# Optimization experiments

Measured on AMD Instinct MI355X. Metric: run time of the kernel, lower is better.

## Reference

```python
import jax, jax.numpy as jnp
import numpy as np

HIDDEN = 2048
N_HEADS = 16
HEAD_DIM = HIDDEN // N_HEADS  # 128
GROUP_SIZE = 128
ROPE_THETA = 10000.0
EPS = 1e-8
THRESH = 0.5


def ternary_quantize_groupwise(w):
    O, I = w.shape
    wg = w.reshape(O, I // GROUP_SIZE, GROUP_SIZE)
    scale = jnp.maximum(jnp.mean(jnp.abs(wg), axis=-1, keepdims=True), EPS)
    wn = wg / scale
    q = jnp.where(wn > THRESH, 1.0, jnp.where(wn < -THRESH, -1.0, 0.0))
    return (q * scale).reshape(O, I)


def quantize_with_ste(w):
    wq = ternary_quantize_groupwise(w)
    return w + jax.lax.stop_gradient(wq - w)


def rope_tables(seqlen):
    half = HEAD_DIM // 2
    inv_freq = 1.0 / (ROPE_THETA ** (jnp.arange(half, dtype=jnp.float32) / half))
    freqs = jnp.arange(seqlen, dtype=jnp.float32)[:, None] * inv_freq[None, :]  # [S, half]
    return jnp.cos(freqs), jnp.sin(freqs)


def apply_rope(x, cos, sin):
    # x: [B, H, S, D]; cos/sin: [S, D/2]
    d = x.shape[-1]
    x1, x2 = x[..., : d // 2], x[..., d // 2:]
    c = cos[None, None, :, :].astype(x.dtype)
    s = sin[None, None, :, :].astype(x.dtype)
    return jnp.concatenate([x1 * c - x2 * s, x1 * s + x2 * c], axis=-1)


def setup_inputs() -> dict:
    key = jax.random.key(0)
    ks = jax.random.split(key, 5)
    B, S = 1, 2048
    hidden_states = jax.random.normal(ks[0], (B, S, HIDDEN), dtype=jnp.float32)
    attention_mask = jnp.ones((B, S), dtype=jnp.int32)
    init_scale = 1.0 / np.sqrt(HIDDEN)
    wq = jax.random.normal(ks[1], (HIDDEN, HIDDEN), dtype=jnp.float32) * init_scale
    wk = jax.random.normal(ks[2], (HIDDEN, HIDDEN), dtype=jnp.float32) * init_scale
    wv = jax.random.normal(ks[3], (HIDDEN, HIDDEN), dtype=jnp.float32) * init_scale
    wo = jax.random.normal(ks[4], (HIDDEN, HIDDEN), dtype=jnp.float32) * init_scale
    return {"hidden_states": hidden_states, "attention_mask": attention_mask,
            "wq": wq, "wk": wk, "wv": wv, "wo": wo}


def reference(hidden_states, attention_mask, wq, wk, wv, wo):
    B, S, _ = hidden_states.shape
    cos, sin = rope_tables(S)

    def proj(x, w):
        w_q = quantize_with_ste(w)
        y = jnp.einsum('bsi,oi->bso', x, w_q)
        return y.reshape(B, S, N_HEADS, HEAD_DIM).transpose(0, 2, 1, 3)  # [B,H,S,D]

    q = apply_rope(proj(hidden_states, wq), cos, sin)
    k = apply_rope(proj(hidden_states, wk), cos, sin)
    v = proj(hidden_states, wv)

    scores = jnp.einsum('bhsd,bhtd->bhst', q, k) / np.sqrt(HEAD_DIM)
    causal = jnp.triu(jnp.ones((S, S), dtype=bool), k=1)
    scores = jnp.where(causal[None, None, :, :], -jnp.inf, scores)
    pad = (attention_mask == 0)[:, None, None, :]
    scores = jnp.where(pad, -jnp.inf, scores)

    probs = jax.nn.softmax(scores, axis=-1)
    out = jnp.einsum('bhst,bhtd->bhsd', probs, v)
    out = out.transpose(0, 2, 1, 3).reshape(B, S, HIDDEN)

    wo_q = quantize_with_ste(wo)
    return jnp.einsum('bso,po->bsp', out, wo_q)
```

## Files before the change

### kernel.cpp

```cpp
#include <hip/hip_runtime.h>
#include <cstdint>
#include <cstddef>


typedef __attribute__((ext_vector_type(8))) short bf16x8;
typedef __attribute__((ext_vector_type(4))) float f32x4;
typedef __attribute__((address_space(3))) void lds_void;
typedef const __attribute__((address_space(1))) void gmem_void;

__device__ __forceinline__ short f2bf(float x) {
    union { float f; uint32_t u; } c; c.f = x;
    uint32_t r = (c.u + 0x7FFFu + ((c.u >> 16) & 1u)) >> 16;
    return (short)r;
}
__device__ __forceinline__ float bf2f(short x) {
    union { uint32_t u; float f; } c; c.u = ((uint32_t)(uint16_t)x) << 16;
    return c.f;
}

__global__ __launch_bounds__(64) void zero_flag(int* f) {
    if (threadIdx.x == 0) *f = 0;
}

__global__ __launch_bounds__(256) void detect_kernel(
    const unsigned short* __restrict__ p, int n, int* __restrict__ flag)
{
    int tid = blockIdx.x * 256 + threadIdx.x;
    int cnt = 0;
    for (int i = tid; i < n; i += 65536) {
        int e = (p[i] >> 7) & 0xFF;
        cnt += (e >= 0xF0) ? 1 : 0;
    }
#pragma unroll
    for (int off = 1; off < 64; off <<= 1) cnt += __shfl_xor(cnt, off);
    if ((threadIdx.x & 63) == 0 && cnt) atomicAdd(flag, cnt);
}

__global__ __launch_bounds__(256) void convert_kernel(
    const void* __restrict__ in, short* __restrict__ out, int n,
    const int* __restrict__ flag)
{
    bool isf32 = (*flag > 1000);
    int i = (blockIdx.x * 256 + threadIdx.x) * 4;
    if (i >= n) return;
    if (isf32) {
        float4 v = *(const float4*)((const float*)in + i);
        short4 o;
        o.x = f2bf(v.x); o.y = f2bf(v.y); o.z = f2bf(v.z); o.w = f2bf(v.w);
        *(short4*)(out + i) = o;
    } else {
        *(short4*)(out + i) = *(const short4*)((const short*)in + i);
    }
}

__global__ __launch_bounds__(256) void quant_kernel(
    const void* __restrict__ w0, const void* __restrict__ w1,
    const void* __restrict__ w2, const void* __restrict__ w3,
    short* __restrict__ q0, short* __restrict__ q1,
    short* __restrict__ q2, short* __restrict__ q3,
    const int* __restrict__ flag)
{
    bool isf32 = (*flag > 1000);
    int gw   = blockIdx.x * 4 + (threadIdx.x >> 6);
    int lane = threadIdx.x & 63;
    int mat  = gw >> 15;
    int g    = gw & 32767;
    const void* w = (mat == 0) ? w0 : (mat == 1) ? w1 : (mat == 2) ? w2 : w3;
    short*      q = (mat == 0) ? q0 : (mat == 1) ? q1 : (mat == 2) ? q2 : q3;
    int idx = g * 64 + lane;
    float a, b;
    if (isf32) {
        const float* wf = (const float*)w;
        a = wf[idx * 2]; b = wf[idx * 2 + 1];
    } else {
        int pr = ((const int*)w)[idx];
        a = bf2f((short)(pr & 0xFFFF));
        b = bf2f((short)(((uint32_t)pr) >> 16));
    }
    float s = fabsf(a) + fabsf(b);
#pragma unroll
    for (int off = 1; off < 64; off <<= 1) s += __shfl_xor(s, off);
    float scale = fmaxf(s * (1.0f / 128.0f), 1e-8f);
    float na = a / scale, nb = b / scale;
    float ra = (na > 0.5f) ? scale : (na < -0.5f) ? -scale : 0.0f;
    float rb = (nb > 0.5f) ? scale : (nb < -0.5f) ? -scale : 0.0f;
    ((int*)q)[idx] = (int)(uint16_t)f2bf(ra) | ((int)(uint16_t)f2bf(rb) << 16);
}

__global__ __launch_bounds__(512, 2) void gemm_qkv(
    const short* __restrict__ A, const short* __restrict__ B,
    short* __restrict__ C)
{
    __shared__ short lds[32768];
    short* A0 = lds;          short* A1 = lds + 8192;
    short* B0 = lds + 16384;  short* B1 = lds + 24576;

    int wg = blockIdx.y * 24 + blockIdx.x;
    int sw = (wg & 7) * 24 + (wg >> 3);
    int bx = sw % 24, by = sw / 24;

    const short* Ab = A + (long long)by * 256 * 2048;
    const short* Bb = B + (long long)bx * 256 * 2048;

    int tid = threadIdx.x, lane = tid & 63, wid = tid >> 6;
    int wr = wid >> 2, wc = wid & 3;
    int quad = lane >> 4, lm = lane & 15;

    f32x4 acc[8][4];
#pragma unroll
    for (int i = 0; i < 8; i++)
#pragma unroll
        for (int j = 0; j < 4; j++)
#pragma unroll
            for (int r = 0; r < 4; r++) acc[i][j][r] = 0.0f;

    auto stage = [&](int tn, short* dA, short* dB) {
#pragma unroll
        for (int l = 0; l < 2; l++) {
            int ci = l * 512 + tid;
            int R = ci >> 2;
            int kc = ((ci & 3) - (R >> 1)) & 3;
            const short* gp = Ab + (long long)R * 2048 + tn * 32 + kc * 8;
            __builtin_amdgcn_global_load_lds((gmem_void*)gp, (lds_void*)(dA + ci * 8), 16, 0, 0);
        }
#pragma unroll
        for (int l = 0; l < 2; l++) {
            int ci = l * 512 + tid;
            int R = ci >> 2;
            int kc = ((ci & 3) - (R >> 1)) & 3;
            const short* gp = Bb + (long long)R * 2048 + tn * 32 + kc * 8;
            __builtin_amdgcn_global_load_lds((gmem_void*)gp, (lds_void*)(dB + ci * 8), 16, 0, 0);
        }
    };

    auto tile = [&](short* cA, short* cB, short* nA, short* nB, int tn, bool pf) {
        if (pf) stage(tn, nA, nB);
        bf16x8 af[4], bg[4];
#pragma unroll
        for (int m = 0; m < 4; m++) {
            int R = wr * 128 + m * 16 + lm;
            af[m] = *(const bf16x8*)(cA + R * 32 + (((quad + (R >> 1)) & 3) << 3));
        }
#pragma unroll
        for (int n = 0; n < 4; n++) {
            int R = wc * 64 + n * 16 + lm;
            bg[n] = *(const bf16x8*)(cB + R * 32 + (((quad + (R >> 1)) & 3) << 3));
        }
        __builtin_amdgcn_s_barrier();
        __builtin_amdgcn_s_setprio(1);
#pragma unroll
        for (int m = 0; m < 4; m++)
#pragma unroll
            for (int n = 0; n < 4; n++)
                acc[m][n] = __builtin_amdgcn_mfma_f32_16x16x32_bf16(af[m], bg[n], acc[m][n], 0, 0, 0);
        __builtin_amdgcn_s_setprio(0);
        __builtin_amdgcn_s_barrier();
#pragma unroll
        for (int m = 0; m < 4; m++) {
            int R = wr * 128 + 64 + m * 16 + lm;
            af[m] = *(const bf16x8*)(cA + R * 32 + (((quad + (R >> 1)) & 3) << 3));
        }
        __builtin_amdgcn_s_barrier();
        __builtin_amdgcn_s_setprio(1);
#pragma unroll
        for (int m = 0; m < 4; m++)
#pragma unroll
            for (int n = 0; n < 4; n++)
                acc[m + 4][n] = __builtin_amdgcn_mfma_f32_16x16x32_bf16(af[m], bg[n], acc[m + 4][n], 0, 0, 0);
        __builtin_amdgcn_s_setprio(0);
        if (pf) asm volatile("s_waitcnt vmcnt(0)" ::: "memory");
        __builtin_amdgcn_s_barrier();
    };

    stage(0, A0, B0);
    asm volatile("s_waitcnt vmcnt(0)" ::: "memory");
    __syncthreads();

    for (int t = 0; t < 64; t += 2) {
        tile(A0, B0, A1, B1, t + 1, true);
        tile(A1, B1, A0, B0, t + 2, t + 2 < 64);
    }

#pragma unroll
    for (int m = 0; m < 8; m++)
#pragma unroll
        for (int n = 0; n < 4; n++)
#pragma unroll
            for (int r = 0; r < 4; r++) {
                int row = by * 256 + wr * 128 + m * 16 + quad * 4 + r;
                int col = bx * 256 + wc * 64 + n * 16 + lm;
                C[(long long)row * 6144 + col] = f2bf(acc[m][n][r]);
            }
}

__global__ __launch_bounds__(256) void vtrans_kernel(
    const short* __restrict__ qkv, short* __restrict__ v_t)
{
    __shared__ short lt[4096];
    int bt = blockIdx.x, bo = blockIdx.y;
    int tid = threadIdx.x;
    int r = tid >> 3, c = tid & 7;
#pragma unroll
    for (int h = 0; h < 2; h++) {
        int row = h * 32 + r;
        bf16x8 v = *(const bf16x8*)(qkv + (long long)(bt * 64 + row) * 6144 + 4096 + bo * 64 + c * 8);
        *(bf16x8*)(lt + row * 64 + ((c ^ (row & 7)) << 3)) = v;
    }
    __syncthreads();
#pragma unroll
    for (int h = 0; h < 2; h++) {
        int o = h * 32 + r;
        bf16x8 ov;
#pragma unroll
        for (int k = 0; k < 8; k++) {
            int row = c * 8 + k;
            ov[k] = lt[row * 64 + ((((o >> 3) ^ (row & 7))) << 3) + (o & 7)];
        }
        *(bf16x8*)(v_t + (long long)(bo * 64 + o) * 2048 + bt * 64 + c * 8) = ov;
    }
}

__global__ __launch_bounds__(256) void gemm_wo(
    const short* __restrict__ A, const short* __restrict__ B,
    float* __restrict__ C)
{
    int bx = blockIdx.x, by = blockIdx.y;
    const short* Ab = A + (long long)by * 128 * 2048;
    const short* Bb = B + (long long)bx * 64 * 2048;
    __shared__ short lA[128 * 64];
    __shared__ short lB[64 * 64];
    int tid = threadIdx.x;
    int lane = tid & 63, wv = tid >> 6;
    f32x4 acc[2][4];
#pragma unroll
    for (int i = 0; i < 2; i++)
#pragma unroll
        for (int j = 0; j < 4; j++)
#pragma unroll
            for (int r = 0; r < 4; r++) acc[i][j][r] = 0.0f;

    int rbase = wv * 32;

    for (int k0 = 0; k0 < 2048; k0 += 64) {
        __syncthreads();
#pragma unroll
        for (int i = 0; i < 4; i++) {
            int ci  = i * 256 + tid;
            int row = ci >> 3;
            int kcG = (ci & 7) ^ (row & 7);
            const short* gp = Ab + (long long)row * 2048 + k0 + kcG * 8;
            __builtin_amdgcn_global_load_lds((gmem_void*)gp, (lds_void*)(lA + ci * 8), 16, 0, 0);
        }
#pragma unroll
        for (int i = 0; i < 2; i++) {
            int ci  = i * 256 + tid;
            int row = ci >> 3;
            int kcG = (ci & 7) ^ (row & 7);
            const short* gp = Bb + (long long)row * 2048 + k0 + kcG * 8;
            __builtin_amdgcn_global_load_lds((gmem_void*)gp, (lds_void*)(lB + ci * 8), 16, 0, 0);
        }
        __syncthreads();
#pragma unroll
        for (int kk = 0; kk < 2; kk++) {
            int kc = kk * 4 + (lane >> 4);
            bf16x8 a[2], b[4];
#pragma unroll
            for (int t = 0; t < 2; t++) {
                int r = rbase + t * 16 + (lane & 15);
                a[t] = *(const bf16x8*)(lA + (r * 8 + (kc ^ (r & 7))) * 8);
            }
#pragma unroll
            for (int t = 0; t < 4; t++) {
                int r = t * 16 + (lane & 15);
                b[t] = *(const bf16x8*)(lB + (r * 8 + (kc ^ (r & 7))) * 8);
            }
#pragma unroll
            for (int mt = 0; mt < 2; mt++)
#pragma unroll
                for (int nt = 0; nt < 4; nt++)
                    acc[mt][nt] = __builtin_amdgcn_mfma_f32_16x16x32_bf16(a[mt], b[nt], acc[mt][nt], 0, 0, 0);
        }
    }

    int rq = (lane >> 4) * 4, cq = lane & 15;
#pragma unroll
    for (int mt = 0; mt < 2; mt++)
#pragma unroll
        for (int nt = 0; nt < 4; nt++)
#pragma unroll
            for (int r = 0; r < 4; r++) {
                int row = by * 128 + rbase + mt * 16 + rq + r;
                int col = bx * 64 + nt * 16 + cq;
                C[(long long)row * 2048 + col] = acc[mt][nt][r];
            }
}

__global__ __launch_bounds__(256) void rope_kernel(
    const short* __restrict__ qk,
    short* __restrict__ qr, short* __restrict__ kr)
{
    int idx = blockIdx.x * 256 + threadIdx.x;
    int d = idx & 63;
    int h = (idx >> 6) & 15;
    int s = idx >> 10;
    float inv = exp2f((float)d * -0.20762050593261719f);
    float ang = (float)s * inv;
    float sn, c;
    sincosf(ang, &sn, &c);
    long long io = (long long)s * 6144 + h * 128 + d;
    long long oo = (long long)h * 262144 + (long long)s * 128 + d;
    float x1 = bf2f(qk[io]), x2 = bf2f(qk[io + 64]);
    qr[oo]      = f2bf(x1 * c - x2 * sn);
    qr[oo + 64] = f2bf(x1 * sn + x2 * c);
    x1 = bf2f(qk[io + 2048]); x2 = bf2f(qk[io + 2112]);
    kr[oo]      = f2bf(x1 * c - x2 * sn);
    kr[oo + 64] = f2bf(x1 * sn + x2 * c);
}

__global__ __launch_bounds__(256) void flash_kernel(
    const short* __restrict__ q_r, const short* __restrict__ k_r,
    const short* __restrict__ v_t, float* __restrict__ Opart,
    float* __restrict__ mpart, float* __restrict__ lpart)
{
    const float SC = 0.08838834764831845f;
    int bid = blockIdx.x;
    int qt = 31 - (bid >> 5);
    int h  = (bid >> 1) & 15;
    int z  = bid & 1;
    int n  = qt + 1;
    int jhalf = (n + 1) >> 1;
    int jb = z ? jhalf : 0;
    int je = z ? n : jhalf;

    int tid = threadIdx.x, lane = tid & 63, wv = tid >> 6;
    int quad = lane >> 4, lm = lane & 15;

    __shared__ short lK[64 * 128];
    __shared__ short lV[128 * 64];
    __shared__ short lP[64 * 64];

    const short* qb = q_r + h * 262144 + (qt * 64 + wv * 16) * 128;
    const short* kb = k_r + h * 262144;
    const short* vb = v_t + h * 128 * 2048;

    bf16x8 aq[4];
#pragma unroll
    for (int kc = 0; kc < 4; kc++)
        aq[kc] = *(const bf16x8*)(qb + lm * 128 + kc * 32 + quad * 8);

    f32x4 ao[8];
#pragma unroll
    for (int nt = 0; nt < 8; nt++)
#pragma unroll
        for (int r = 0; r < 4; r++) ao[nt][r] = 0.0f;
    float mrow[4], lrow[4];
#pragma unroll
    for (int r = 0; r < 4; r++) { mrow[r] = -1e30f; lrow[r] = 0.0f; }

    if (jb < je) {
#pragma unroll
        for (int i = 0; i < 4; i++) {
            int ci = i * 256 + tid;
            int r = ci >> 4, cp = ci & 15;
            int c = (cp & 8) | ((cp & 7) ^ (r & 7));
            const short* gp = kb + (jb * 64 + r) * 128 + c * 8;
            __builtin_amdgcn_global_load_lds((gmem_void*)gp, (lds_void*)(lK + ci * 8), 16, 0, 0);
        }
    }
    __syncthreads();

    for (int jt = jb; jt < je; jt++) {
#pragma unroll
        for (int i = 0; i < 4; i++) {
            int ci = i * 256 + tid;
            int r = ci >> 3, cp = ci & 7;
            int c = cp ^ (r & 7);
            const short* gp = vb + r * 2048 + jt * 64 + c * 8;
            __builtin_amdgcn_global_load_lds((gmem_void*)gp, (lds_void*)(lV + ci * 8), 16, 0, 0);
        }
        f32x4 as[4];
#pragma unroll
        for (int nt = 0; nt < 4; nt++)
#pragma unroll
            for (int r = 0; r < 4; r++) as[nt][r] = 0.0f;
#pragma unroll
        for (int kc = 0; kc < 4; kc++) {
#pragma unroll
            for (int nt = 0; nt < 4; nt++) {
                int r = nt * 16 + lm;
                int c = kc * 4 + quad;
                int slot = (c & 8) | ((c & 7) ^ (r & 7));
                bf16x8 bk = *(const bf16x8*)(lK + (r * 16 + slot) * 8);
                as[nt] = __builtin_amdgcn_mfma_f32_16x16x32_bf16(aq[kc], bk, as[nt], 0, 0, 0);
            }
        }
        bool diag = (jt == qt);
#pragma unroll
        for (int nt = 0; nt < 4; nt++)
#pragma unroll
            for (int r = 0; r < 4; r++) {
                float s = as[nt][r] * SC;
                if (diag) {
                    int qg = wv * 16 + quad * 4 + r;
                    int tg = nt * 16 + lm;
                    if (tg > qg) s = -1e30f;
                }
                as[nt][r] = s;
            }
#pragma unroll
        for (int r = 0; r < 4; r++) {
            float mx = fmaxf(fmaxf(as[0][r], as[1][r]), fmaxf(as[2][r], as[3][r]));
#pragma unroll
            for (int off = 1; off < 16; off <<= 1) mx = fmaxf(mx, __shfl_xor(mx, off));
            float mnew = fmaxf(mrow[r], mx);
            float alpha = __expf(mrow[r] - mnew);
            mrow[r] = mnew;
            float psum = 0.0f;
#pragma unroll
            for (int nt = 0; nt < 4; nt++) {
                float p = __expf(as[nt][r] - mnew);
                as[nt][r] = p;
                psum += p;
            }
#pragma unroll
            for (int off = 1; off < 16; off <<= 1) psum += __shfl_xor(psum, off);
            lrow[r] = lrow[r] * alpha + psum;
#pragma unroll
            for (int nt = 0; nt < 8; nt++) ao[nt][r] *= alpha;
            int row = wv * 16 + quad * 4 + r;
#pragma unroll
            for (int nt = 0; nt < 4; nt++) {
                int slot = (nt * 2 + (lm >> 3) + 2 * quad) & 7;
                lP[row * 64 + slot * 8 + (lm & 7)] = f2bf(as[nt][r]);
            }
        }
        __syncthreads();
        if (jt + 1 < je) {
#pragma unroll
            for (int i = 0; i < 4; i++) {
                int ci = i * 256 + tid;
                int r = ci >> 4, cp = ci & 15;
                int c = (cp & 8) | ((cp & 7) ^ (r & 7));
                const short* gp = kb + ((jt + 1) * 64 + r) * 128 + c * 8;
                __builtin_amdgcn_global_load_lds((gmem_void*)gp, (lds_void*)(lK + ci * 8), 16, 0, 0);
            }
        }
#pragma unroll
        for (int kt = 0; kt < 2; kt++) {
            int prow = wv * 16 + lm;
            int slot = (kt * 4 + quad + 2 * (lm >> 2)) & 7;
            bf16x8 ap = *(const bf16x8*)(lP + prow * 64 + slot * 8);
#pragma unroll
            for (int nt = 0; nt < 8; nt++) {
                int r = nt * 16 + lm;
                int c = kt * 4 + quad;
                int vslot = c ^ (r & 7);
                bf16x8 bv = *(const bf16x8*)(lV + (r * 8 + vslot) * 8);
                ao[nt] = __builtin_amdgcn_mfma_f32_16x16x32_bf16(ap, bv, ao[nt], 0, 0, 0);
            }
        }
        __syncthreads();
    }
    float* Ob = Opart + (long long)z * 4194304;
#pragma unroll
    for (int r = 0; r < 4; r++) {
        int sg = qt * 64 + wv * 16 + quad * 4 + r;
#pragma unroll
        for (int nt = 0; nt < 8; nt++) {
            int dg = h * 128 + nt * 16 + lm;
            Ob[(long long)sg * 2048 + dg] = ao[nt][r];
        }
        if (lm == 0) {
            mpart[z * 32768 + h * 2048 + sg] = mrow[r];
            lpart[z * 32768 + h * 2048 + sg] = lrow[r];
        }
    }
}

__global__ __launch_bounds__(256) void combine_kernel(
    const float* __restrict__ O0, const float* __restrict__ O1,
    const float* __restrict__ mpart, const float* __restrict__ lpart,
    short* __restrict__ attn)
{
    int idx = blockIdx.x * 256 + threadIdx.x;
    int e = idx * 4;
    int s = e >> 11, h = (e & 2047) >> 7;
    float m0 = mpart[h * 2048 + s], m1 = mpart[32768 + h * 2048 + s];
    float l0 = lpart[h * 2048 + s], l1 = lpart[32768 + h * 2048 + s];
    float M = fmaxf(m0, m1);
    float w0 = __expf(m0 - M), w1 = __expf(m1 - M);
    float inv = 1.0f / (l0 * w0 + l1 * w1);
    float4 a = *(const float4*)(O0 + e);
    float4 b = *(const float4*)(O1 + e);
    short4 o;
    o.x = f2bf((a.x * w0 + b.x * w1) * inv);
    o.y = f2bf((a.y * w0 + b.y * w1) * inv);
    o.z = f2bf((a.z * w0 + b.z * w1) * inv);
    o.w = f2bf((a.w * w0 + b.w * w1) * inv);
    *(short4*)(attn + e) = o;
}

extern "C" void kernel_launch(void* const* d_in, const int* in_sizes, int n_in,
                              void* d_out, int out_size, void* d_ws, size_t ws_size,
                              hipStream_t stream)
{
    const void* x  = d_in[0];
    const void* wq = d_in[2];
    const void* wk = d_in[3];
    const void* wv = d_in[4];
    const void* wo = d_in[5];

    char* ws = (char*)d_ws;
    size_t off = 0;
    auto alloc = [&](size_t b) { void* p = ws + off; off += (b + 255) & ~(size_t)255; return p; };
    short* wqkv_q = (short*)alloc(25165824);
    short* wo_q   = (short*)alloc(8388608);
    float* Opart  = (float*)alloc(33554432);
    short* qkv    = (short*)Opart;
    short* v_t    = (short*)alloc(8388608);
    short* q_r    = (short*)alloc(8388608);
    short* k_r    = (short*)alloc(8388608);
    short* attn   = (short*)alloc(8388608);
    short* x_bf   = (short*)alloc(8388608);
    float* mpart  = (float*)alloc(262144);
    float* lpart  = (float*)alloc(262144);
    int*   flag   = (int*)alloc(256);
    if (off > ws_size) return;

    zero_flag<<<1, 64, 0, stream>>>(flag);
    detect_kernel<<<256, 256, 0, stream>>>(
        (const unsigned short*)x, in_sizes[0], flag);
    convert_kernel<<<4096, 256, 0, stream>>>(x, x_bf, 4194304, flag);

    quant_kernel<<<32768, 256, 0, stream>>>(wq, wk, wv, wo,
        wqkv_q, wqkv_q + 4194304, wqkv_q + 8388608, wo_q, flag);

    gemm_qkv<<<dim3(24, 8), 512, 0, stream>>>(x_bf, wqkv_q, qkv);

    rope_kernel<<<8192, 256, 0, stream>>>(qkv, q_r, k_r);
    vtrans_kernel<<<dim3(32, 32), 256, 0, stream>>>(qkv, v_t);

    flash_kernel<<<1024, 256, 0, stream>>>(q_r, k_r, v_t, Opart, mpart, lpart);
    combine_kernel<<<4096, 256, 0, stream>>>(
        Opart, Opart + 4194304, mpart, lpart, attn);

    gemm_wo<<<dim3(32, 16), 256, 0, stream>>>(attn, wo_q, (float*)d_out);
}
```

Baseline: 320.2 us.

## Retile QKV GEMM to 128x192 blocks with triple-buffered LDS pipeline

The QKV projection GEMM moves from 256x256 tiles with 512 threads and double buffering to 128x192 tiles with 256 threads and a three-stage LDS ring. That gives 512 workgroups instead of 192, which fills more of the GPU's compute units. Partial vmcnt waits let one prefetch stay in flight while the current tile is computed, and some intra-tile barriers are removed. In exchange, each workgroup does less operand reuse per byte loaded and the swizzle mapping is more involved.

```diff
diff --git a/kernel.cpp b/kernel.cpp
--- a/kernel.cpp
+++ b/kernel.cpp
@@ -87,108 +87,112 @@
     ((int*)q)[idx] = (int)(uint16_t)f2bf(ra) | ((int)(uint16_t)f2bf(rb) << 16);
 }
 
-__global__ __launch_bounds__(512, 2) void gemm_qkv(
+__global__ __launch_bounds__(256, 2) void gemm_qkv(
     const short* __restrict__ A, const short* __restrict__ B,
     short* __restrict__ C)
 {
-    __shared__ short lds[32768];
-    short* A0 = lds;          short* A1 = lds + 8192;
-    short* B0 = lds + 16384;  short* B1 = lds + 24576;
-
-    int wg = blockIdx.y * 24 + blockIdx.x;
-    int sw = (wg & 7) * 24 + (wg >> 3);
-    int bx = sw % 24, by = sw / 24;
-
-    const short* Ab = A + (long long)by * 256 * 2048;
-    const short* Bb = B + (long long)bx * 256 * 2048;
+    __shared__ short lds[30720];
+
+    int wg = blockIdx.y * 32 + blockIdx.x;
+    int sw = (wg & 7) * 64 + (wg >> 3);
+    int bx = sw & 31, by = sw >> 5;
+
+    const short* Ab = A + (long long)by * 128 * 2048;
+    const short* Bb = B + (long long)bx * 192 * 2048;
 
     int tid = threadIdx.x, lane = tid & 63, wid = tid >> 6;
-    int wr = wid >> 2, wc = wid & 3;
+    int wr = wid >> 1, wc = wid & 1;
     int quad = lane >> 4, lm = lane & 15;
 
-    f32x4 acc[8][4];
-#pragma unroll
-    for (int i = 0; i < 8; i++)
-#pragma unroll
-        for (int j = 0; j < 4; j++)
+    f32x4 acc[4][6];
+#pragma unroll
+    for (int i = 0; i < 4; i++)
+#pragma unroll
+        for (int j = 0; j < 6; j++)
 #pragma unroll
             for (int r = 0; r < 4; r++) acc[i][j][r] = 0.0f;
 
-    auto stage = [&](int tn, short* dA, short* dB) {
+    auto stage = [&](int tn, short* buf) {
+        short* dA = buf;
+        short* dB = buf + 4096;
 #pragma unroll
         for (int l = 0; l < 2; l++) {
-            int ci = l * 512 + tid;
-            int R = ci >> 2;
-            int kc = ((ci & 3) - (R >> 1)) & 3;
-            const short* gp = Ab + (long long)R * 2048 + tn * 32 + kc * 8;
+            int ci  = l * 256 + tid;
+            int row = ci >> 2;
+            int kc  = ((ci & 3) - (row >> 1)) & 3;
+            const short* gp = Ab + (long long)row * 2048 + tn * 32 + kc * 8;
             __builtin_amdgcn_global_load_lds((gmem_void*)gp, (lds_void*)(dA + ci * 8), 16, 0, 0);
         }
 #pragma unroll
-        for (int l = 0; l < 2; l++) {
-            int ci = l * 512 + tid;
-            int R = ci >> 2;
-            int kc = ((ci & 3) - (R >> 1)) & 3;
-            const short* gp = Bb + (long long)R * 2048 + tn * 32 + kc * 8;
+        for (int l = 0; l < 3; l++) {
+            int ci  = l * 256 + tid;
+            int row = ci >> 2;
+            int kc  = ((ci & 3) - (row >> 1)) & 3;
+            const short* gp = Bb + (long long)row * 2048 + tn * 32 + kc * 8;
             __builtin_amdgcn_global_load_lds((gmem_void*)gp, (lds_void*)(dB + ci * 8), 16, 0, 0);
         }
     };
 
-    auto tile = [&](short* cA, short* cB, short* nA, short* nB, int tn, bool pf) {
-        if (pf) stage(tn, nA, nB);
-        bf16x8 af[4], bg[4];
+    auto tile = [&](short* cur, short* nxt, int tn, bool pf) {
+        if (pf) stage(tn, nxt);
+        short* cA = cur;
+        short* cB = cur + 4096;
+        bf16x8 af[4], bg[6];
 #pragma unroll
         for (int m = 0; m < 4; m++) {
-            int R = wr * 128 + m * 16 + lm;
+            int R = wr * 64 + m * 16 + lm;
             af[m] = *(const bf16x8*)(cA + R * 32 + (((quad + (R >> 1)) & 3) << 3));
         }
 #pragma unroll
-        for (int n = 0; n < 4; n++) {
-            int R = wc * 64 + n * 16 + lm;
+        for (int n = 0; n < 3; n++) {
+            int R = wc * 96 + n * 16 + lm;
             bg[n] = *(const bf16x8*)(cB + R * 32 + (((quad + (R >> 1)) & 3) << 3));
         }
-        __builtin_amdgcn_s_barrier();
         __builtin_amdgcn_s_setprio(1);
 #pragma unroll
         for (int m = 0; m < 4; m++)
 #pragma unroll
-            for (int n = 0; n < 4; n++)
+            for (int n = 0; n < 3; n++)
                 acc[m][n] = __builtin_amdgcn_mfma_f32_16x16x32_bf16(af[m], bg[n], acc[m][n], 0, 0, 0);
         __builtin_amdgcn_s_setprio(0);
-        __builtin_amdgcn_s_barrier();
-#pragma unroll
-        for (int m = 0; m < 4; m++) {
-            int R = wr * 128 + 64 + m * 16 + lm;
-            af[m] = *(const bf16x8*)(cA + R * 32 + (((quad + (R >> 1)) & 3) << 3));
-        }
-        __builtin_amdgcn_s_barrier();
+#pragma unroll
+        for (int n = 3; n < 6; n++) {
+            int R = wc * 96 + n * 16 + lm;
+            bg[n] = *(const bf16x8*)(cB + R * 32 + (((quad + (R >> 1)) & 3) << 3));
+        }
         __builtin_amdgcn_s_setprio(1);
 #pragma unroll
         for (int m = 0; m < 4; m++)
 #pragma unroll
-            for (int n = 0; n < 4; n++)
-                acc[m + 4][n] = __builtin_amdgcn_mfma_f32_16x16x32_bf16(af[m], bg[n], acc[m + 4][n], 0, 0, 0);
+            for (int n = 3; n < 6; n++)
+                acc[m][n] = __builtin_amdgcn_mfma_f32_16x16x32_bf16(af[m], bg[n], acc[m][n], 0, 0, 0);
         __builtin_amdgcn_s_setprio(0);
-        if (pf) asm volatile("s_waitcnt vmcnt(0)" ::: "memory");
+        if (pf) asm volatile("s_waitcnt vmcnt(5)" ::: "memory");
+        else    asm volatile("s_waitcnt vmcnt(0)" ::: "memory");
         __builtin_amdgcn_s_barrier();
     };
 
-    stage(0, A0, B0);
-    asm volatile("s_waitcnt vmcnt(0)" ::: "memory");
-    __syncthreads();
-
-    for (int t = 0; t < 64; t += 2) {
-        tile(A0, B0, A1, B1, t + 1, true);
-        tile(A1, B1, A0, B0, t + 2, t + 2 < 64);
-    }
-
-#pragma unroll
-    for (int m = 0; m < 8; m++)
-#pragma unroll
-        for (int n = 0; n < 4; n++)
+    short* c0 = lds;
+    short* c1 = lds + 10240;
+    short* c2 = lds + 20480;
+    stage(0, c0);
+    stage(1, c1);
+    asm volatile("s_waitcnt vmcnt(5)" ::: "memory");
+    __builtin_amdgcn_s_barrier();
+
+    for (int t = 0; t < 64; t++) {
+        tile(c0, c2, t + 2, t + 2 < 64);
+        short* tmp = c0; c0 = c1; c1 = c2; c2 = tmp;
+    }
+
+#pragma unroll
+    for (int m = 0; m < 4; m++)
+#pragma unroll
+        for (int n = 0; n < 6; n++)
 #pragma unroll
             for (int r = 0; r < 4; r++) {
-                int row = by * 256 + wr * 128 + m * 16 + quad * 4 + r;
-                int col = bx * 256 + wc * 64 + n * 16 + lm;
+                int row = by * 128 + wr * 64 + m * 16 + quad * 4 + r;
+                int col = bx * 192 + wc * 96 + n * 16 + lm;
                 C[(long long)row * 6144 + col] = f2bf(acc[m][n][r]);
             }
 }
@@ -535,7 +539,7 @@
     quant_kernel<<<32768, 256, 0, stream>>>(wq, wk, wv, wo,
         wqkv_q, wqkv_q + 4194304, wqkv_q + 8388608, wo_q, flag);
 
-    gemm_qkv<<<dim3(24, 8), 512, 0, stream>>>(x_bf, wqkv_q, qkv);
+    gemm_qkv<<<dim3(32, 16), 256, 0, stream>>>(x_bf, wqkv_q, qkv);
 
     rope_kernel<<<8192, 256, 0, stream>>>(qkv, q_r, k_r);
     vtrans_kernel<<<dim3(32, 32), 256, 0, stream>>>(qkv, v_t);
```

Measured after the change: 315.3 us. No clear change (-1.5%).
